# Kernel tuning notes

Hardware: AMD Instinct MI355X
Metric: run time of the kernel (lower is better)

Reference implementation:

```python
import jax, jax.numpy as jnp
import numpy as np

TEMPERATURE = 0.07
EPS = 1e-8  # torch CosineSimilarity norm clamp

N, D, NUM_CLASSES = 4096, 768, 128


def setup_inputs() -> dict:
    key = jax.random.key(0)
    k1, k2, k3 = jax.random.split(key, 3)
    img_emb = jax.random.normal(k1, (N, D), dtype=jnp.float32)
    text_emb = jax.random.normal(k2, (N, D), dtype=jnp.float32)
    labels = jax.random.randint(k3, (N,), 0, NUM_CLASSES, dtype=jnp.int64)
    return {"img_emb": img_emb, "text_emb": text_emb, "labels": labels}


def reference(img_emb, text_emb, labels):
    # cosine similarity via normalize + matmul (avoids O(N^2 D) broadcast)
    img_n = img_emb / jnp.maximum(jnp.linalg.norm(img_emb, axis=-1, keepdims=True), EPS)
    txt_n = text_emb / jnp.maximum(jnp.linalg.norm(text_emb, axis=-1, keepdims=True), EPS)
    logits = jnp.einsum('id,jd->ij', img_n, txt_n) / TEMPERATURE  # [N, N]

    pos_mask = (labels[:, None] == labels[None, :]).astype(logits.dtype)  # [N, N]

    img2text = -(pos_mask * jax.nn.log_softmax(logits, axis=1)).sum(1).mean()
    text2img = -(pos_mask * jax.nn.log_softmax(logits, axis=0)).sum(0).mean()
    return (img2text + text2img) / 2
```

## Files before the change

### kernel.cpp

```cpp
#include <hip/hip_runtime.h>
#include <hip/hip_bf16.h>

#define N_ 4096
#define D_ 768
#define NCLS 128
#define BM 128
#define BN 128
#define BKB 128
#define NSTEP 6

typedef float f32x4 __attribute__((ext_vector_type(4)));
typedef long lng2 __attribute__((ext_vector_type(2)));

#define SBAR() asm volatile("s_barrier" ::: "memory")
#define VMWAIT8() asm volatile("s_waitcnt vmcnt(8)" ::: "memory")
#define LGKM0() asm volatile("s_waitcnt lgkmcnt(0)" ::: "memory")

__device__ __forceinline__ void gload16(const unsigned char* g, unsigned char* l) {
  __builtin_amdgcn_global_load_lds(
      (const __attribute__((address_space(1))) unsigned int*)g,
      (__attribute__((address_space(3))) unsigned int*)l, 16, 0, 0);
}

__global__ __launch_bounds__(192) void normalize_kernel(
    const float* __restrict__ img, const float* __restrict__ txt,
    unsigned char* __restrict__ img_f8, unsigned char* __restrict__ txt_f8,
    double* __restrict__ accs, unsigned* __restrict__ cnt) {
  int b = blockIdx.x;
  if (b == 0 && threadIdx.x == 0) {
    accs[0] = 0.0;
    accs[1] = 0.0;
    *cnt = 0u;
  }
  const float* s;
  unsigned char* d;
  if (b < N_) {
    s = img + (size_t)b * D_;
    d = img_f8 + (size_t)b * D_;
  } else {
    s = txt + (size_t)(b - N_) * D_;
    d = txt_f8 + (size_t)(b - N_) * D_;
  }
  int tid = threadIdx.x;
  float4 v = ((const float4*)s)[tid];
  float ss = v.x * v.x + v.y * v.y + v.z * v.z + v.w * v.w;
#pragma unroll
  for (int m = 32; m; m >>= 1) ss += __shfl_xor(ss, m);
  __shared__ float wsum[3];
  int lane = tid & 63, w = tid >> 6;
  if (lane == 0) wsum[w] = ss;
  __syncthreads();
  float inv = 1.0f / fmaxf(sqrtf(wsum[0] + wsum[1] + wsum[2]), 1e-8f);
  int r = 0;
  r = __builtin_amdgcn_cvt_pk_fp8_f32(v.x * inv, v.y * inv, r, false);
  r = __builtin_amdgcn_cvt_pk_fp8_f32(v.z * inv, v.w * inv, r, true);
  const int k0 = tid * 4;
  const int seg = k0 >> 7, ko = k0 & 127;
  const int ks = ko >> 5, gg = (ko >> 3) & 3, h = (ko >> 2) & 1;
  ((int*)d)[seg * 32 + (gg * 2 + (ks >> 1)) * 4 + (ks & 1) * 2 + h] = r;
}

__global__ __launch_bounds__(256) void gemm_epi_kernel(
    const unsigned char* __restrict__ A, const unsigned char* __restrict__ B,
    const int* __restrict__ labels, float* __restrict__ row_part,
    float* __restrict__ col_part, float* __restrict__ S_part) {
  __shared__ __align__(16) unsigned char As[2][16384];
  __shared__ __align__(16) unsigned char Bs[2][16384];
  __shared__ int labR[BM], labC[BN];
  __shared__ float rbuf[2][BM], cbuf[2][BN];
  __shared__ float sbuf[4];

  const int lin = blockIdx.y * 32 + blockIdx.x;
  const int xcd = lin & 7, idx = lin >> 3;
  const int bx = xcd * 4 + (idx & 3), by = idx >> 2;

  const int tid = threadIdx.x;
  const int lane = tid & 63, wave = tid >> 6;
  const int wr = wave >> 1, wc = wave & 1;
  const int g = lane >> 4, fr = lane & 15;
  const int rowBase = by * BM, colBase = bx * BN;

  if (tid < BM) labR[tid] = labels[rowBase + tid];
  else labC[tid - BM] = labels[colBase + tid - BM];
  __syncthreads();

  const int r0 = lane >> 3;
  const int cswz = (lane & 7) ^ (r0 & 7);
  const unsigned char* pa = A + (size_t)(rowBase + wave * 8 + r0) * D_ + cswz * 16;
  const unsigned char* pb = B + (size_t)(colBase + wave * 8 + r0) * D_ + cswz * 16;
  const int dbase = wave * 1024;

#pragma unroll
  for (int j = 0; j < 4; ++j) {
    gload16(pa + (size_t)(32 * j) * D_, &As[0][dbase + j * 4096]);
    gload16(pb + (size_t)(32 * j) * D_, &Bs[0][dbase + j * 4096]);
  }

  f32x4 acc[4][4] = {};

  for (int u = 0; u < NSTEP; ++u) {
    SBAR();
    {
      const int su = (u + 1 < NSTEP) ? u + 1 : u;
      const size_t kk = (size_t)su * BKB;
      const int sl = (u + 1) & 1;
#pragma unroll
      for (int j = 0; j < 4; ++j) {
        gload16(pa + (size_t)(32 * j) * D_ + kk, &As[sl][dbase + j * 4096]);
        gload16(pb + (size_t)(32 * j) * D_ + kk, &Bs[sl][dbase + j * 4096]);
      }
    }
    VMWAIT8();
    SBAR();
    const unsigned char* as_ = As[u & 1];
    const unsigned char* bs_ = Bs[u & 1];
#pragma unroll
    for (int p = 0; p < 2; ++p) {
      const int gp = g * 2 + p;
      lng2 bq[4];
#pragma unroll
      for (int n = 0; n < 4; ++n) {
        const int row = wc * 64 + n * 16 + fr;
        bq[n] = *(const lng2*)&bs_[row * 128 + (gp ^ (fr & 7)) * 16];
      }
#pragma unroll
      for (int m = 0; m < 4; ++m) {
        const int row = wr * 64 + m * 16 + fr;
        lng2 aq = *(const lng2*)&as_[row * 128 + (gp ^ (fr & 7)) * 16];
#pragma unroll
        for (int n = 0; n < 4; ++n) {
          acc[m][n] = __builtin_amdgcn_mfma_f32_16x16x32_fp8_fp8(aq[0], bq[n][0], acc[m][n], 0, 0, 0);
          acc[m][n] = __builtin_amdgcn_mfma_f32_16x16x32_fp8_fp8(aq[1], bq[n][1], acc[m][n], 0, 0, 0);
        }
      }
    }
    LGKM0();
  }
  __syncthreads();

  const float scale = 14.285714285714286f;
  float sPart = 0.f;
  float colAcc[4] = {0.f, 0.f, 0.f, 0.f};
#pragma unroll
  for (int m = 0; m < 4; ++m) {
    float ra2[4] = {0.f, 0.f, 0.f, 0.f};
#pragma unroll
    for (int n = 0; n < 4; ++n) {
      int col = wc * 64 + n * 16 + fr;
      int lc = labC[col];
#pragma unroll
      for (int r = 0; r < 4; ++r) {
        float v = acc[m][n][r] * scale;
        float e = __expf(v);
        ra2[r] += e;
        colAcc[n] += e;
        int row = wr * 64 + m * 16 + g * 4 + r;
        if (labR[row] == lc) sPart += v;
      }
    }
#pragma unroll
    for (int r = 0; r < 4; ++r) {
      float x = ra2[r];
      x += __shfl_xor(x, 1);
      x += __shfl_xor(x, 2);
      x += __shfl_xor(x, 4);
      x += __shfl_xor(x, 8);
      if (fr == 0) rbuf[wc][wr * 64 + m * 16 + g * 4 + r] = x;
    }
  }
#pragma unroll
  for (int n = 0; n < 4; ++n) {
    float x = colAcc[n];
    x += __shfl_xor(x, 16);
    x += __shfl_xor(x, 32);
    if (g == 0) cbuf[wr][wc * 64 + n * 16 + fr] = x;
  }
  float s = sPart;
#pragma unroll
  for (int m = 32; m; m >>= 1) s += __shfl_xor(s, m);
  if (lane == 0) sbuf[wave] = s;
  __syncthreads();
  if (tid < BM)
    row_part[(size_t)bx * N_ + rowBase + tid] = rbuf[0][tid] + rbuf[1][tid];
  else
    col_part[(size_t)by * N_ + colBase + (tid - BM)] = cbuf[0][tid - BM] + cbuf[1][tid - BM];
  if (tid == 0) S_part[by * 32 + bx] = sbuf[0] + sbuf[1] + sbuf[2] + sbuf[3];
}

__global__ __launch_bounds__(256) void reduce_kernel(
    const float* __restrict__ row_part, const float* __restrict__ col_part,
    const float* __restrict__ S_part, const int* __restrict__ labels,
    double* __restrict__ accs, unsigned* __restrict__ cnt, float* __restrict__ out) {
  __shared__ int hist[NCLS];
  int tid = threadIdx.x;
  if (tid < NCLS) hist[tid] = 0;
  __syncthreads();
  for (int j = tid; j < N_; j += 256) atomicAdd(&hist[labels[j]], 1);
  __syncthreads();

  int i = blockIdx.x * 256 + tid;
  float rs = 0.f, cs = 0.f;
#pragma unroll
  for (int b = 0; b < 32; ++b) {
    rs += row_part[(size_t)b * N_ + i];
    cs += col_part[(size_t)b * N_ + i];
  }
  int c = hist[labels[i]];
  double term = (double)c * ((double)logf(rs) + (double)logf(cs));
  double sterm = (i < 1024) ? (double)S_part[i] : 0.0;
#pragma unroll
  for (int m = 32; m; m >>= 1) {
    term += __shfl_xor(term, m);
    sterm += __shfl_xor(sterm, m);
  }
  __shared__ double tbuf[4], sb[4];
  int lane = tid & 63, w = tid >> 6;
  if (lane == 0) { tbuf[w] = term; sb[w] = sterm; }
  __syncthreads();
  if (tid == 0) {
    atomicAdd(&accs[0], tbuf[0] + tbuf[1] + tbuf[2] + tbuf[3]);
    atomicAdd(&accs[1], sb[0] + sb[1] + sb[2] + sb[3]);
    __threadfence();
    unsigned old = atomicAdd(cnt, 1u);
    if (old == 15u) {
      double t = atomicAdd(&accs[0], 0.0);
      double s2 = atomicAdd(&accs[1], 0.0);
      out[0] = (float)((t - 2.0 * s2) / (2.0 * (double)N_));
    }
  }
}

extern "C" void kernel_launch(void* const* d_in, const int* in_sizes, int n_in,
                              void* d_out, int out_size, void* d_ws, size_t ws_size,
                              hipStream_t stream) {
  const float* img = (const float*)d_in[0];
  const float* txt = (const float*)d_in[1];
  const int* labels = (const int*)d_in[2];
  float* out = (float*)d_out;
  char* ws = (char*)d_ws;

  unsigned char* img_f8 = (unsigned char*)(ws);
  unsigned char* txt_f8 = (unsigned char*)(ws + 3145728);
  float* row_part = (float*)(ws + 6291456);
  float* col_part = (float*)(ws + 6815744);
  float* S_part = (float*)(ws + 7340032);
  double* accs = (double*)(ws + 7344128);
  unsigned* cnt = (unsigned*)(ws + 7344144);

  normalize_kernel<<<2 * N_, 192, 0, stream>>>(img, txt, img_f8, txt_f8, accs, cnt);
  gemm_epi_kernel<<<dim3(32, 32), 256, 0, stream>>>(
      img_f8, txt_f8, labels, row_part, col_part, S_part);
  reduce_kernel<<<16, 256, 0, stream>>>(row_part, col_part, S_part, labels, accs, cnt, out);
}
```

Before: 46.19 us.

## Fuse final reduction into GEMM epilogue via atomics and last-block finalize

Drops the separate reduce kernel. Each GEMM block now atomically adds its row and column exp-sums into global N-length arrays and its positive-logit sum into a double accumulator. The last block to finish, found with an atomic counter, builds the label histogram and computes the final loss. This removes one kernel launch and the partial-sum buffers, at the cost of float atomic contention, a single block doing the whole final pass over 4096 rows, and nondeterministic summation order.

```diff
diff --git a/kernel.cpp b/kernel.cpp
--- a/kernel.cpp
+++ b/kernel.cpp
@@ -8,6 +8,7 @@
 #define BN 128
 #define BKB 128
 #define NSTEP 6
+#define NBLK 1024
 
 typedef float f32x4 __attribute__((ext_vector_type(4)));
 typedef long lng2 __attribute__((ext_vector_type(2)));
@@ -25,12 +26,15 @@
 __global__ __launch_bounds__(192) void normalize_kernel(
     const float* __restrict__ img, const float* __restrict__ txt,
     unsigned char* __restrict__ img_f8, unsigned char* __restrict__ txt_f8,
-    double* __restrict__ accs, unsigned* __restrict__ cnt) {
+    float* __restrict__ sums, double* __restrict__ accs, unsigned* __restrict__ cnt) {
   int b = blockIdx.x;
-  if (b == 0 && threadIdx.x == 0) {
-    accs[0] = 0.0;
-    accs[1] = 0.0;
-    *cnt = 0u;
+  if (threadIdx.x == 0) {
+    sums[b] = 0.f;
+    if (b == 0) {
+      accs[0] = 0.0;
+      accs[1] = 0.0;
+      *cnt = 0u;
+    }
   }
   const float* s;
   unsigned char* d;
@@ -62,13 +66,15 @@
 
 __global__ __launch_bounds__(256) void gemm_epi_kernel(
     const unsigned char* __restrict__ A, const unsigned char* __restrict__ B,
-    const int* __restrict__ labels, float* __restrict__ row_part,
-    float* __restrict__ col_part, float* __restrict__ S_part) {
+    const int* __restrict__ labels, float* __restrict__ row_sum,
+    float* __restrict__ col_sum, double* __restrict__ accs,
+    unsigned* __restrict__ cnt, float* __restrict__ out) {
   __shared__ __align__(16) unsigned char As[2][16384];
   __shared__ __align__(16) unsigned char Bs[2][16384];
   __shared__ int labR[BM], labC[BN];
   __shared__ float rbuf[2][BM], cbuf[2][BN];
   __shared__ float sbuf[4];
+  __shared__ unsigned oldv;
 
   const int lin = blockIdx.y * 32 + blockIdx.x;
   const int xcd = lin & 7, idx = lin >> 3;
@@ -181,49 +187,36 @@
   if (lane == 0) sbuf[wave] = s;
   __syncthreads();
   if (tid < BM)
-    row_part[(size_t)bx * N_ + rowBase + tid] = rbuf[0][tid] + rbuf[1][tid];
+    atomicAdd(&row_sum[rowBase + tid], rbuf[0][tid] + rbuf[1][tid]);
   else
-    col_part[(size_t)by * N_ + colBase + (tid - BM)] = cbuf[0][tid - BM] + cbuf[1][tid - BM];
-  if (tid == 0) S_part[by * 32 + bx] = sbuf[0] + sbuf[1] + sbuf[2] + sbuf[3];
-}
-
-__global__ __launch_bounds__(256) void reduce_kernel(
-    const float* __restrict__ row_part, const float* __restrict__ col_part,
-    const float* __restrict__ S_part, const int* __restrict__ labels,
-    double* __restrict__ accs, unsigned* __restrict__ cnt, float* __restrict__ out) {
-  __shared__ int hist[NCLS];
-  int tid = threadIdx.x;
-  if (tid < NCLS) hist[tid] = 0;
-  __syncthreads();
-  for (int j = tid; j < N_; j += 256) atomicAdd(&hist[labels[j]], 1);
-  __syncthreads();
-
-  int i = blockIdx.x * 256 + tid;
-  float rs = 0.f, cs = 0.f;
-#pragma unroll
-  for (int b = 0; b < 32; ++b) {
-    rs += row_part[(size_t)b * N_ + i];
-    cs += col_part[(size_t)b * N_ + i];
-  }
-  int c = hist[labels[i]];
-  double term = (double)c * ((double)logf(rs) + (double)logf(cs));
-  double sterm = (i < 1024) ? (double)S_part[i] : 0.0;
-#pragma unroll
-  for (int m = 32; m; m >>= 1) {
-    term += __shfl_xor(term, m);
-    sterm += __shfl_xor(sterm, m);
-  }
-  __shared__ double tbuf[4], sb[4];
-  int lane = tid & 63, w = tid >> 6;
-  if (lane == 0) { tbuf[w] = term; sb[w] = sterm; }
+    atomicAdd(&col_sum[colBase + (tid - BM)], cbuf[0][tid - BM] + cbuf[1][tid - BM]);
+  if (tid == 0)
+    atomicAdd(&accs[1], (double)(sbuf[0] + sbuf[1] + sbuf[2] + sbuf[3]));
   __syncthreads();
   if (tid == 0) {
-    atomicAdd(&accs[0], tbuf[0] + tbuf[1] + tbuf[2] + tbuf[3]);
-    atomicAdd(&accs[1], sb[0] + sb[1] + sb[2] + sb[3]);
     __threadfence();
-    unsigned old = atomicAdd(cnt, 1u);
-    if (old == 15u) {
-      double t = atomicAdd(&accs[0], 0.0);
+    oldv = atomicAdd(cnt, 1u);
+  }
+  __syncthreads();
+  if (oldv == NBLK - 1) {
+    __shared__ int hist[NCLS];
+    __shared__ double tbuf[4];
+    if (tid < NCLS) hist[tid] = 0;
+    __syncthreads();
+    for (int j = tid; j < N_; j += 256) atomicAdd(&hist[labels[j]], 1);
+    __syncthreads();
+    double term = 0.0;
+    for (int i = tid; i < N_; i += 256) {
+      float rs = atomicAdd(&row_sum[i], 0.f);
+      float cs = atomicAdd(&col_sum[i], 0.f);
+      term += (double)hist[labels[i]] * ((double)logf(rs) + (double)logf(cs));
+    }
+#pragma unroll
+    for (int m = 32; m; m >>= 1) term += __shfl_xor(term, m);
+    if (lane == 0) tbuf[wave] = term;
+    __syncthreads();
+    if (tid == 0) {
+      double t = tbuf[0] + tbuf[1] + tbuf[2] + tbuf[3];
       double s2 = atomicAdd(&accs[1], 0.0);
       out[0] = (float)((t - 2.0 * s2) / (2.0 * (double)N_));
     }
@@ -241,14 +234,13 @@
 
   unsigned char* img_f8 = (unsigned char*)(ws);
   unsigned char* txt_f8 = (unsigned char*)(ws + 3145728);
-  float* row_part = (float*)(ws + 6291456);
-  float* col_part = (float*)(ws + 6815744);
-  float* S_part = (float*)(ws + 7340032);
-  double* accs = (double*)(ws + 7344128);
-  unsigned* cnt = (unsigned*)(ws + 7344144);
-
-  normalize_kernel<<<2 * N_, 192, 0, stream>>>(img, txt, img_f8, txt_f8, accs, cnt);
+  float* sums = (float*)(ws + 6291456);
+  float* row_sum = sums;
+  float* col_sum = sums + N_;
+  double* accs = (double*)(ws + 6324224);
+  unsigned* cnt = (unsigned*)(ws + 6324240);
+
+  normalize_kernel<<<2 * N_, 192, 0, stream>>>(img, txt, img_f8, txt_f8, sums, accs, cnt);
   gemm_epi_kernel<<<dim3(32, 32), 256, 0, stream>>>(
-      img_f8, txt_f8, labels, row_part, col_part, S_part);
-  reduce_kernel<<<16, 256, 0, stream>>>(row_part, col_part, S_part, labels, accs, cnt, out);
-}
+      img_f8, txt_f8, labels, row_sum, col_sum, accs, cnt, out);
+}
```

Measured after the change: 67.91 us. +47.0%, slower.
